# Kernel tuning notes

Measured on AMD Instinct MI355X. Metric: run time of the kernel, lower is better.

The kernel has to match this reference:

```python
import jax, jax.numpy as jnp
import numpy as np

NUM_DISPARITIES = 64


def setup_inputs() -> dict:
    key = jax.random.key(0)
    k1, k2 = jax.random.split(key)
    B, C, H, W = 4, 32, 256, 512
    left = jax.random.normal(k1, (B, C, H, W), dtype=jnp.float32)
    right = jax.random.normal(k2, (B, C, H, W), dtype=jnp.float32)
    return {"left": left, "right": right}


def cost_volume(left, right, num_disparities):
    # left, right: [B, C, H, W] -> output [B, D, H, W]
    W = left.shape[3]
    wcoord = jnp.arange(W)  # [W]

    def one_disparity(i):
        # right shifted so rs[..., w] == right[..., w - i] for w >= i
        rs = jnp.roll(right, i, axis=3)
        corr = jnp.mean(left * rs, axis=1)  # [B, H, W] channel-mean dot product
        # zero out invalid columns w < i (matches zeros-init + slice write in torch)
        return jnp.where(wcoord >= i, corr, jnp.zeros_like(corr))

    # sequential map over disparities keeps peak memory at one [B,C,H,W] product
    out = jax.lax.map(one_disparity, jnp.arange(num_disparities))  # [D, B, H, W]
    return jnp.transpose(out, (1, 0, 2, 3))  # [B, D, H, W]


def reference(left, right):
    return cost_volume(left, right, NUM_DISPARITIES)
```

## Files before the change

### kernel.cpp

```cpp
#include <hip/hip_runtime.h>


constexpr int Bn = 4, Cn = 32, Hn = 256, Wn = 512, Dn = 64;
constexpr int WT = 4, DT = 16;
constexpr int PAD = 64;
constexpr int STRIDE = PAD + Wn;
constexpr int HW = Hn * Wn;

__global__ __launch_bounds__(512, 4)
void cost_volume_kernel(const float* __restrict__ left,
                        const float* __restrict__ right,
                        float* __restrict__ out)
{
    __shared__ __align__(16) float Rs[Cn * STRIDE];

    const int tid = threadIdx.x;
    const int bh  = blockIdx.x;
    const int b   = bh >> 8;
    const int h   = bh & (Hn - 1);

    const float* Lrow = left  + (b * Cn * Hn + h) * Wn;
    const float* Rrow = right + (b * Cn * Hn + h) * Wn;

    {
        const int c  = tid >> 4;
        const int wq = (tid & 15) << 2;
        *reinterpret_cast<float4*>(&Rs[c * STRIDE + wq]) =
            make_float4(0.f, 0.f, 0.f, 0.f);
    }

    #pragma unroll
    for (int k = 0; k < 8; ++k) {
        const int f = tid + (k << 9);
        const int c = f >> 7;
        const int w = (f & 127) << 2;
        const float4 v = *reinterpret_cast<const float4*>(&Rrow[c * HW + w]);
        *reinterpret_cast<float4*>(&Rs[c * STRIDE + PAD + w]) = v;
    }
    __syncthreads();

    const int tw = tid & 127;
    const int td = tid >> 7;
    const int w0 = tw << 2;
    const int d0 = td << 4;
    const int rbase = PAD + w0 - d0 - 16;

    float acc[DT][WT];
    #pragma unroll
    for (int j = 0; j < DT; ++j)
        #pragma unroll
        for (int i = 0; i < WT; ++i)
            acc[j][i] = 0.f;

    for (int c = 0; c < Cn; ++c) {
        const float4 Lv = *reinterpret_cast<const float4*>(&Lrow[c * HW + w0]);
        const float lv[4] = {Lv.x, Lv.y, Lv.z, Lv.w};

        const float* rp = &Rs[c * STRIDE + rbase];
        float r[20];
        #pragma unroll
        for (int q = 0; q < 5; ++q)
            *reinterpret_cast<float4*>(&r[q * 4]) =
                *reinterpret_cast<const float4*>(&rp[q * 4]);

        #pragma unroll
        for (int j = 0; j < DT; ++j)
            #pragma unroll
            for (int i = 0; i < WT; ++i)
                acc[j][i] = fmaf(lv[i], r[16 + i - j], acc[j][i]);
    }

    constexpr float inv = 1.0f / 32.0f;
    float* op = out + ((b * Dn + d0) * Hn + h) * Wn + w0;
    #pragma unroll
    for (int j = 0; j < DT; ++j) {
        const float4 v = make_float4(acc[j][0] * inv, acc[j][1] * inv,
                                     acc[j][2] * inv, acc[j][3] * inv);
        *reinterpret_cast<float4*>(&op[j * HW]) = v;
    }
}

extern "C" void kernel_launch(void* const* d_in, const int* in_sizes, int n_in,
                              void* d_out, int out_size, void* d_ws, size_t ws_size,
                              hipStream_t stream) {
    const float* left  = (const float*)d_in[0];
    const float* right = (const float*)d_in[1];
    float* out = (float*)d_out;
    cost_volume_kernel<<<dim3(Bn * Hn), dim3(512), 0, stream>>>(left, right, out);
}
```

Baseline: 249.8 us.

## Split disparities across two blocks, chunk channels in LDS, async global-to-LDS loads

Each (b,h) row is now handled by two blocks, each covering 32 disparities, so every thread accumulates 8 instead of 16 disparities. The right-image row is staged into LDS in two 16-channel chunks using global_load_lds direct copies, which halves the LDS footprint and allows higher occupancy (launch bounds raised to 8). The cost is that left and right rows are read from global memory twice and an extra barrier is added per chunk.

```diff
diff --git a/kernel.cpp b/kernel.cpp
--- a/kernel.cpp
+++ b/kernel.cpp
@@ -2,48 +2,41 @@
 
 
 constexpr int Bn = 4, Cn = 32, Hn = 256, Wn = 512, Dn = 64;
-constexpr int WT = 4, DT = 16;
+constexpr int CCH = 16;
+constexpr int WT = 4, DT = 8;
 constexpr int PAD = 64;
 constexpr int STRIDE = PAD + Wn;
 constexpr int HW = Hn * Wn;
 
-__global__ __launch_bounds__(512, 4)
+__global__ __launch_bounds__(512, 8)
 void cost_volume_kernel(const float* __restrict__ left,
                         const float* __restrict__ right,
                         float* __restrict__ out)
 {
-    __shared__ __align__(16) float Rs[Cn * STRIDE];
+    __shared__ __align__(16) float Rs[CCH * STRIDE];
 
-    const int tid = threadIdx.x;
-    const int bh  = blockIdx.x;
-    const int b   = bh >> 8;
-    const int h   = bh & (Hn - 1);
+    const int tid  = threadIdx.x;
+    const int bid  = blockIdx.x;
+    const int dblk = bid & 1;
+    const int bh   = bid >> 1;
+    const int b    = bh >> 8;
+    const int h    = bh & (Hn - 1);
 
     const float* Lrow = left  + (b * Cn * Hn + h) * Wn;
     const float* Rrow = right + (b * Cn * Hn + h) * Wn;
 
-    {
+    if (tid < CCH * (PAD / 4)) {
         const int c  = tid >> 4;
         const int wq = (tid & 15) << 2;
         *reinterpret_cast<float4*>(&Rs[c * STRIDE + wq]) =
             make_float4(0.f, 0.f, 0.f, 0.f);
     }
 
-    #pragma unroll
-    for (int k = 0; k < 8; ++k) {
-        const int f = tid + (k << 9);
-        const int c = f >> 7;
-        const int w = (f & 127) << 2;
-        const float4 v = *reinterpret_cast<const float4*>(&Rrow[c * HW + w]);
-        *reinterpret_cast<float4*>(&Rs[c * STRIDE + PAD + w]) = v;
-    }
-    __syncthreads();
-
     const int tw = tid & 127;
     const int td = tid >> 7;
     const int w0 = tw << 2;
-    const int d0 = td << 4;
-    const int rbase = PAD + w0 - d0 - 16;
+    const int d0 = (dblk << 5) + (td << 3);
+    const int rbase = PAD + w0 - d0 - 8;
 
     float acc[DT][WT];
     #pragma unroll
@@ -52,22 +45,41 @@
         for (int i = 0; i < WT; ++i)
             acc[j][i] = 0.f;
 
-    for (int c = 0; c < Cn; ++c) {
-        const float4 Lv = *reinterpret_cast<const float4*>(&Lrow[c * HW + w0]);
-        const float lv[4] = {Lv.x, Lv.y, Lv.z, Lv.w};
-
-        const float* rp = &Rs[c * STRIDE + rbase];
-        float r[20];
-        #pragma unroll
-        for (int q = 0; q < 5; ++q)
-            *reinterpret_cast<float4*>(&r[q * 4]) =
-                *reinterpret_cast<const float4*>(&rp[q * 4]);
+    for (int cc = 0; cc < Cn; cc += CCH) {
+        if (cc) __syncthreads();
 
         #pragma unroll
-        for (int j = 0; j < DT; ++j)
+        for (int k = 0; k < 4; ++k) {
+            const int f = tid + (k << 9);
+            const int c = f >> 7;
+            const int w = (f & 127) << 2;
+            __builtin_amdgcn_global_load_lds(
+                (const __attribute__((address_space(1))) void*)(Rrow + (cc + c) * HW + w),
+                (__attribute__((address_space(3))) void*)(&Rs[c * STRIDE + PAD + w]),
+                16, 0, 0);
+        }
+        __syncthreads();
+
+        #pragma unroll 2
+        for (int c = 0; c < CCH; ++c) {
+            const float4 Lv =
+                *reinterpret_cast<const float4*>(&Lrow[(cc + c) * HW + w0]);
+
+            const float* rp = &Rs[c * STRIDE + rbase];
+            float r[12];
             #pragma unroll
-            for (int i = 0; i < WT; ++i)
-                acc[j][i] = fmaf(lv[i], r[16 + i - j], acc[j][i]);
+            for (int q = 0; q < 3; ++q)
+                *reinterpret_cast<float4*>(&r[q * 4]) =
+                    *reinterpret_cast<const float4*>(&rp[q * 4]);
+
+            #pragma unroll
+            for (int j = 0; j < DT; ++j) {
+                acc[j][0] = fmaf(Lv.x, r[8 - j],  acc[j][0]);
+                acc[j][1] = fmaf(Lv.y, r[9 - j],  acc[j][1]);
+                acc[j][2] = fmaf(Lv.z, r[10 - j], acc[j][2]);
+                acc[j][3] = fmaf(Lv.w, r[11 - j], acc[j][3]);
+            }
+        }
     }
 
     constexpr float inv = 1.0f / 32.0f;
@@ -86,5 +98,5 @@
     const float* left  = (const float*)d_in[0];
     const float* right = (const float*)d_in[1];
     float* out = (float*)d_out;
-    cost_volume_kernel<<<dim3(Bn * Hn), dim3(512), 0, stream>>>(left, right, out);
+    cost_volume_kernel<<<dim3(Bn * Hn * 2), dim3(512), 0, stream>>>(left, right, out);
 }
```

Result: slower. 266.6 us (+6.7%).

## Double-buffer channel chunks of left/right rows in LDS via async global_load_lds

Applied to the files above, without the earlier changes.

Replaces the single up-front load of all 32 right-image channels into shared memory with a double-buffered pipeline over 8-channel chunks. Both the left and right rows are copied into LDS with direct global-to-LDS loads, so the next chunk is fetched while the current one is computed. Left values now come from LDS instead of per-channel global loads. This adds per-chunk barriers and depends on the async LDS loads being complete before each barrier.

```diff
diff --git a/kernel.cpp b/kernel.cpp
--- a/kernel.cpp
+++ b/kernel.cpp
@@ -2,17 +2,21 @@
 
 
 constexpr int Bn = 4, Cn = 32, Hn = 256, Wn = 512, Dn = 64;
+constexpr int CCH = 8;
 constexpr int WT = 4, DT = 16;
 constexpr int PAD = 64;
 constexpr int STRIDE = PAD + Wn;
 constexpr int HW = Hn * Wn;
+constexpr int RBUF = CCH * STRIDE;
+constexpr int LBUF = CCH * Wn;
 
 __global__ __launch_bounds__(512, 4)
 void cost_volume_kernel(const float* __restrict__ left,
                         const float* __restrict__ right,
                         float* __restrict__ out)
 {
-    __shared__ __align__(16) float Rs[Cn * STRIDE];
+    __shared__ __align__(16) float Rs[2][RBUF];
+    __shared__ __align__(16) float Ls[2][LBUF];
 
     const int tid = threadIdx.x;
     const int bh  = blockIdx.x;
@@ -22,22 +26,30 @@
     const float* Lrow = left  + (b * Cn * Hn + h) * Wn;
     const float* Rrow = right + (b * Cn * Hn + h) * Wn;
 
-    {
-        const int c  = tid >> 4;
+    if (tid < 2 * CCH * (PAD / 4)) {
+        const int s  = tid >> 7;
+        const int c  = (tid >> 4) & (CCH - 1);
         const int wq = (tid & 15) << 2;
-        *reinterpret_cast<float4*>(&Rs[c * STRIDE + wq]) =
+        *reinterpret_cast<float4*>(&Rs[s][c * STRIDE + wq]) =
             make_float4(0.f, 0.f, 0.f, 0.f);
     }
 
-    #pragma unroll
-    for (int k = 0; k < 8; ++k) {
-        const int f = tid + (k << 9);
-        const int c = f >> 7;
-        const int w = (f & 127) << 2;
-        const float4 v = *reinterpret_cast<const float4*>(&Rrow[c * HW + w]);
-        *reinterpret_cast<float4*>(&Rs[c * STRIDE + PAD + w]) = v;
-    }
-    __syncthreads();
+    auto stage = [&](int sel, int cc) {
+        #pragma unroll
+        for (int k = 0; k < 2; ++k) {
+            const int f = tid + (k << 9);
+            const int c = f >> 7;
+            const int w = (f & 127) << 2;
+            __builtin_amdgcn_global_load_lds(
+                (const __attribute__((address_space(1))) void*)(Rrow + (cc + c) * HW + w),
+                (__attribute__((address_space(3))) void*)(&Rs[sel][c * STRIDE + PAD + w]),
+                16, 0, 0);
+            __builtin_amdgcn_global_load_lds(
+                (const __attribute__((address_space(1))) void*)(Lrow + (cc + c) * HW + w),
+                (__attribute__((address_space(3))) void*)(&Ls[sel][c * Wn + w]),
+                16, 0, 0);
+        }
+    };
 
     const int tw = tid & 127;
     const int td = tid >> 7;
@@ -52,22 +64,39 @@
         for (int i = 0; i < WT; ++i)
             acc[j][i] = 0.f;
 
-    for (int c = 0; c < Cn; ++c) {
-        const float4 Lv = *reinterpret_cast<const float4*>(&Lrow[c * HW + w0]);
-        const float lv[4] = {Lv.x, Lv.y, Lv.z, Lv.w};
+    stage(0, 0);
 
-        const float* rp = &Rs[c * STRIDE + rbase];
-        float r[20];
-        #pragma unroll
-        for (int q = 0; q < 5; ++q)
-            *reinterpret_cast<float4*>(&r[q * 4]) =
-                *reinterpret_cast<const float4*>(&rp[q * 4]);
+    int sel = 0;
+    for (int cc = 0; cc < Cn; cc += CCH) {
+        __syncthreads();
 
-        #pragma unroll
-        for (int j = 0; j < DT; ++j)
+        if (cc + CCH < Cn)
+            stage(sel ^ 1, cc + CCH);
+
+        const float* Rb = &Rs[sel][0];
+        const float* Lb = &Ls[sel][0];
+
+        #pragma unroll 2
+        for (int c = 0; c < CCH; ++c) {
+            const float4 Lv =
+                *reinterpret_cast<const float4*>(&Lb[c * Wn + w0]);
+
+            const float* rp = &Rb[c * STRIDE + rbase];
+            float r[20];
             #pragma unroll
-            for (int i = 0; i < WT; ++i)
-                acc[j][i] = fmaf(lv[i], r[16 + i - j], acc[j][i]);
+            for (int q = 0; q < 5; ++q)
+                *reinterpret_cast<float4*>(&r[q * 4]) =
+                    *reinterpret_cast<const float4*>(&rp[q * 4]);
+
+            #pragma unroll
+            for (int j = 0; j < DT; ++j) {
+                acc[j][0] = fmaf(Lv.x, r[16 - j], acc[j][0]);
+                acc[j][1] = fmaf(Lv.y, r[17 - j], acc[j][1]);
+                acc[j][2] = fmaf(Lv.z, r[18 - j], acc[j][2]);
+                acc[j][3] = fmaf(Lv.w, r[19 - j], acc[j][3]);
+            }
+        }
+        sel ^= 1;
     }
 
     constexpr float inv = 1.0f / 32.0f;
```

After: 244.9 us. No clear change (-1.9%).

## Restructure into single-wave blocks with async global-to-LDS channel pipeline

Applied to the files above, without the earlier changes.

Each block is now a single 64-lane wavefront covering a quarter of a row (half of W by half of D), with 32x4 accumulators per lane. Instead of staging all 32 channels of right into shared memory behind a block barrier, a 4-slot ring buffer is filled with direct global-to-LDS loads of right and left per channel. Explicit vmcnt waits overlap the loads with the FMA work of earlier channels. This removes the __syncthreads and the upfront staging stall and reduces LDS footprint, at the cost of higher register pressure and redundant loads of right across the four blocks per row.

```diff
diff --git a/kernel.cpp b/kernel.cpp
--- a/kernel.cpp
+++ b/kernel.cpp
@@ -2,78 +2,106 @@
 
 
 constexpr int Bn = 4, Cn = 32, Hn = 256, Wn = 512, Dn = 64;
-constexpr int WT = 4, DT = 16;
+constexpr int HW  = Hn * Wn;
 constexpr int PAD = 64;
-constexpr int STRIDE = PAD + Wn;
-constexpr int HW = Hn * Wn;
+constexpr int SLOTR = PAD + Wn;
+constexpr int SLOTL = 256;
+constexpr int SLOT  = SLOTR + SLOTL;
+constexpr int NBUF  = 4;
 
-__global__ __launch_bounds__(512, 4)
+__global__ __launch_bounds__(64, 2)
 void cost_volume_kernel(const float* __restrict__ left,
                         const float* __restrict__ right,
                         float* __restrict__ out)
 {
-    __shared__ __align__(16) float Rs[Cn * STRIDE];
+    __shared__ __align__(16) float Buf[NBUF][SLOT];
 
-    const int tid = threadIdx.x;
-    const int bh  = blockIdx.x;
-    const int b   = bh >> 8;
-    const int h   = bh & (Hn - 1);
+    const int lane = threadIdx.x;
+    const int row  = blockIdx.x;
+    const int quad = blockIdx.y;
+    const int wh   = (quad & 1) << 8;
+    const int dh   = (quad >> 1) << 5;
+    const int b    = row >> 8;
+    const int h    = row & (Hn - 1);
 
     const float* Lrow = left  + (b * Cn * Hn + h) * Wn;
     const float* Rrow = right + (b * Cn * Hn + h) * Wn;
 
     {
-        const int c  = tid >> 4;
-        const int wq = (tid & 15) << 2;
-        *reinterpret_cast<float4*>(&Rs[c * STRIDE + wq]) =
-            make_float4(0.f, 0.f, 0.f, 0.f);
+        const int s = lane >> 4;
+        const int o = (lane & 15) << 2;
+        *reinterpret_cast<float4*>(&Buf[s][o]) = make_float4(0.f, 0.f, 0.f, 0.f);
     }
 
+    const int l4 = lane << 2;
+
+    auto stage = [&](int slot, int c) {
+        const float* rsrc = Rrow + c * HW + l4;
+        __builtin_amdgcn_global_load_lds(
+            (const __attribute__((address_space(1))) void*)rsrc,
+            (__attribute__((address_space(3))) void*)&Buf[slot][PAD + l4],
+            16, 0, 0);
+        __builtin_amdgcn_global_load_lds(
+            (const __attribute__((address_space(1))) void*)(rsrc + 256),
+            (__attribute__((address_space(3))) void*)&Buf[slot][PAD + 256 + l4],
+            16, 0, 0);
+        __builtin_amdgcn_global_load_lds(
+            (const __attribute__((address_space(1))) void*)(Lrow + c * HW + wh + l4),
+            (__attribute__((address_space(3))) void*)&Buf[slot][SLOTR + l4],
+            16, 0, 0);
+    };
+
+    stage(0, 0);
+    stage(1, 1);
+    stage(2, 2);
+
+    float acc[32][4];
     #pragma unroll
-    for (int k = 0; k < 8; ++k) {
-        const int f = tid + (k << 9);
-        const int c = f >> 7;
-        const int w = (f & 127) << 2;
-        const float4 v = *reinterpret_cast<const float4*>(&Rrow[c * HW + w]);
-        *reinterpret_cast<float4*>(&Rs[c * STRIDE + PAD + w]) = v;
-    }
-    __syncthreads();
-
-    const int tw = tid & 127;
-    const int td = tid >> 7;
-    const int w0 = tw << 2;
-    const int d0 = td << 4;
-    const int rbase = PAD + w0 - d0 - 16;
-
-    float acc[DT][WT];
-    #pragma unroll
-    for (int j = 0; j < DT; ++j)
+    for (int j = 0; j < 32; ++j)
         #pragma unroll
-        for (int i = 0; i < WT; ++i)
+        for (int i = 0; i < 4; ++i)
             acc[j][i] = 0.f;
 
-    for (int c = 0; c < Cn; ++c) {
-        const float4 Lv = *reinterpret_cast<const float4*>(&Lrow[c * HW + w0]);
-        const float lv[4] = {Lv.x, Lv.y, Lv.z, Lv.w};
+    const int rbase = PAD + wh + l4 - dh - 32;
 
-        const float* rp = &Rs[c * STRIDE + rbase];
-        float r[20];
+    auto compute = [&](int c) {
+        const float* Sb = &Buf[c & (NBUF - 1)][0];
+        const float4 Lv = *reinterpret_cast<const float4*>(&Sb[SLOTR + l4]);
+        float r[40];
         #pragma unroll
-        for (int q = 0; q < 5; ++q)
+        for (int q = 0; q < 10; ++q)
             *reinterpret_cast<float4*>(&r[q * 4]) =
-                *reinterpret_cast<const float4*>(&rp[q * 4]);
+                *reinterpret_cast<const float4*>(&Sb[rbase + q * 4]);
+        #pragma unroll
+        for (int j = 0; j < 32; ++j) {
+            acc[j][0] = fmaf(Lv.x, r[32 - j], acc[j][0]);
+            acc[j][1] = fmaf(Lv.y, r[33 - j], acc[j][1]);
+            acc[j][2] = fmaf(Lv.z, r[34 - j], acc[j][2]);
+            acc[j][3] = fmaf(Lv.w, r[35 - j], acc[j][3]);
+        }
+    };
 
-        #pragma unroll
-        for (int j = 0; j < DT; ++j)
-            #pragma unroll
-            for (int i = 0; i < WT; ++i)
-                acc[j][i] = fmaf(lv[i], r[16 + i - j], acc[j][i]);
+    for (int c = 0; c < Cn - 3; ++c) {
+        __builtin_amdgcn_sched_barrier(0);
+        stage((c + 3) & (NBUF - 1), c + 3);
+        asm volatile("s_waitcnt vmcnt(9)" ::: "memory");
+        __builtin_amdgcn_sched_barrier(0);
+        compute(c);
     }
+    asm volatile("s_waitcnt vmcnt(6)" ::: "memory");
+    __builtin_amdgcn_sched_barrier(0);
+    compute(Cn - 3);
+    asm volatile("s_waitcnt vmcnt(3)" ::: "memory");
+    __builtin_amdgcn_sched_barrier(0);
+    compute(Cn - 2);
+    asm volatile("s_waitcnt vmcnt(0)" ::: "memory");
+    __builtin_amdgcn_sched_barrier(0);
+    compute(Cn - 1);
 
     constexpr float inv = 1.0f / 32.0f;
-    float* op = out + ((b * Dn + d0) * Hn + h) * Wn + w0;
+    float* op = out + ((b * Dn + dh) * Hn + h) * Wn + wh + l4;
     #pragma unroll
-    for (int j = 0; j < DT; ++j) {
+    for (int j = 0; j < 32; ++j) {
         const float4 v = make_float4(acc[j][0] * inv, acc[j][1] * inv,
                                      acc[j][2] * inv, acc[j][3] * inv);
         *reinterpret_cast<float4*>(&op[j * HW]) = v;
@@ -86,5 +114,5 @@
     const float* left  = (const float*)d_in[0];
     const float* right = (const float*)d_in[1];
     float* out = (float*)d_out;
-    cost_volume_kernel<<<dim3(Bn * Hn), dim3(512), 0, stream>>>(left, right, out);
+    cost_volume_kernel<<<dim3(Bn * Hn, 4), dim3(64), 0, stream>>>(left, right, out);
 }
```

After: 257.5 us. 1.03x slower.
